# Performance work log

Hardware: AMD Instinct MI355X
Metric: run time of the kernel (lower is better)

Reference implementation:

```python
import jax, jax.numpy as jnp
import numpy as np

N_NODES = 100000
N_EDGES = 3200000
D_FEAT = 128
N1 = 128
N2 = 64
NUM_CLASSES = 10
NUM_GRAPHS = 256


def gcn_conv(x, edge_index, W, b, num_nodes):
    """PyG GCNConv: y = D^-1/2 (A+I) D^-1/2 (x W) + b, self-loops added."""
    src, dst = edge_index[0], edge_index[1]
    # degree including self-loop (edge weight 1)
    deg = jax.ops.segment_sum(jnp.ones_like(dst, dtype=x.dtype), dst,
                              num_segments=num_nodes) + 1.0
    dis = jnp.where(deg > 0, deg ** -0.5, 0.0)  # deg_inv_sqrt, [N]
    h = x @ W                                    # transform first, [N, out]
    norm = dis[src] * dis[dst]                   # [E]
    msg = h[src] * norm[:, None]                 # gather + scale, [E, out]
    agg = jax.ops.segment_sum(msg, dst, num_segments=num_nodes)
    agg = agg + h * (dis * dis)[:, None]         # self-loop contribution
    return agg + b


def global_mean_pool(x, batch, num_graphs):
    sums = jax.ops.segment_sum(x, batch, num_segments=num_graphs)
    cnt = jax.ops.segment_sum(jnp.ones((x.shape[0],), dtype=x.dtype), batch,
                              num_segments=num_graphs)
    return sums / jnp.maximum(cnt, 1.0)[:, None]


def setup_inputs() -> dict:
    key = jax.random.key(0)
    ks = jax.random.split(key, 8)
    x = jax.random.normal(ks[0], (N_NODES, D_FEAT), dtype=jnp.float32)
    edge_index = jax.random.randint(ks[1], (2, N_EDGES), 0, N_NODES, dtype=jnp.int64)
    batch = jnp.sort(jax.random.randint(ks[2], (N_NODES,), 0, NUM_GRAPHS, dtype=jnp.int64))
    W1 = jax.random.normal(ks[3], (D_FEAT, N1), dtype=jnp.float32) / np.sqrt(D_FEAT)
    b1 = jnp.zeros((N1,), dtype=jnp.float32)
    W2 = jax.random.normal(ks[4], (N1, N2), dtype=jnp.float32) / np.sqrt(N1)
    b2 = jnp.zeros((N2,), dtype=jnp.float32)
    Wfc = jax.random.normal(ks[5], (N2, NUM_CLASSES), dtype=jnp.float32) / np.sqrt(N2)
    bfc = jnp.zeros((NUM_CLASSES,), dtype=jnp.float32)
    return {"x": x, "edge_index": edge_index, "batch": batch,
            "W1": W1, "b1": b1, "W2": W2, "b2": b2,
            "Wfc": Wfc, "bfc": bfc, "num_graphs": NUM_GRAPHS}


def reference(x, edge_index, batch, W1, b1, W2, b2, Wfc, bfc, num_graphs):
    n = x.shape[0]
    h = gcn_conv(x, edge_index, W1, b1, n)
    h = jax.nn.relu(h)
    h = gcn_conv(h, edge_index, W2, b2, n)
    g = global_mean_pool(h, batch, num_graphs)   # [num_graphs, N2]
    # dropout is identity at inference
    return g @ Wfc + bfc                          # [num_graphs, num_classes]
```

## Files before the change

kernel.cpp:

```cpp
#include <hip/hip_runtime.h>
#include <math.h>

typedef unsigned int  u32;
typedef unsigned short u16;

#define TILE1 8192
#define BKW   256
#define CAP   9216

typedef __attribute__((ext_vector_type(8))) short bf16x8;
typedef __attribute__((ext_vector_type(4))) float f32x4;
union frag_u { bf16x8 v; u32 u[4]; uint4 q; };

__device__ inline u32 bf16_rne(float f) {
    u32 u = __float_as_uint(f);
    return (u + 0x7FFFu + ((u >> 16) & 1u)) >> 16;
}
__device__ inline float bf_lo(u32 u) { return __uint_as_float(u << 16); }
__device__ inline float bf_hi(u32 u) { return __uint_as_float(u & 0xFFFF0000u); }

__device__ inline void add8(float* acc, uint4 q) {
    acc[0] += bf_lo(q.x); acc[1] += bf_hi(q.x);
    acc[2] += bf_lo(q.y); acc[3] += bf_hi(q.y);
    acc[4] += bf_lo(q.z); acc[5] += bf_hi(q.z);
    acc[6] += bf_lo(q.w); acc[7] += bf_hi(q.w);
}

__device__ inline u32 relu_pk(u32 v) {
    u32 s = v & 0x80008000u;
    u32 m = (s >> 15) * 0xFFFFu;
    return v & ~m;
}


__global__ __launch_bounds__(512) void k_part1(const int* __restrict__ ei,
                                               int* __restrict__ bucketCur,
                                               u32* __restrict__ tmp,
                                               int E, int N, int NBK) {
    __shared__ int hist[1024];
    __shared__ int base[512];
    const int tid = threadIdx.x;
    if (tid < NBK) { hist[tid] = 0; hist[512 + tid] = 0; }
    __syncthreads();

    const int rep = (tid & 1) << 9;
    const int t0 = blockIdx.x * TILE1;
    const int4* ei4s = (const int4*)ei;
    const int4* ei4d = (const int4*)(ei + E);
    const int q0 = t0 >> 2;
    const int QE = E >> 2;

    int sv[16], dv[16], key[16];
#pragma unroll
    for (int j = 0; j < 4; ++j) {
        int qi = q0 + j * 512 + tid;
        int4 s4 = make_int4(0, 0, 0, 0), d4 = make_int4(-1, -1, -1, -1);
        if (qi < QE) { s4 = ei4s[qi]; d4 = ei4d[qi]; }
        sv[4 * j + 0] = s4.x; dv[4 * j + 0] = d4.x;
        sv[4 * j + 1] = s4.y; dv[4 * j + 1] = d4.y;
        sv[4 * j + 2] = s4.z; dv[4 * j + 2] = d4.z;
        sv[4 * j + 3] = s4.w; dv[4 * j + 3] = d4.w;
    }
#pragma unroll
    for (int j = 0; j < 16; ++j) {
        key[j] = -1;
        if ((unsigned)dv[j] < (unsigned)N && (unsigned)sv[j] < (unsigned)N) {
            key[j] = dv[j] >> 8;
            atomicAdd(&hist[key[j] + rep], 1);
        }
    }
    __syncthreads();
    if (tid < NBK) {
        int tot = hist[tid] + hist[512 + tid];
        base[tid] = atomicAdd(&bucketCur[tid], tot);
        hist[tid] = 0;
    }
    __syncthreads();
#pragma unroll
    for (int j = 0; j < 16; ++j) {
        if (key[j] >= 0) {
            int slot = atomicAdd(&hist[key[j]], 1);
            int off = base[key[j]] + slot;
            if (off < CAP)
                tmp[(size_t)key[j] * CAP + off] =
                    ((u32)(dv[j] & 255) << 17) | (u32)sv[j];
        }
    }
}

__global__ __launch_bounds__(512) void k_part2(const int* __restrict__ bucketCnt,
                                               const u32* __restrict__ tmp,
                                               int* __restrict__ csr,
                                               int* __restrict__ rowptr,
                                               float* __restrict__ dis,
                                               int N, int NBK) {
    __shared__ int hist[256];
    __shared__ int ts[512];
    __shared__ int sStart;
    const int b = blockIdx.x;
    const int t = threadIdx.x;

    int myCnt = (t < NBK) ? bucketCnt[t] : 0;
    ts[t] = myCnt;
    __syncthreads();
    for (int off = 1; off < 512; off <<= 1) {
        int u = (t >= off) ? ts[t - off] : 0;
        __syncthreads();
        ts[t] += u;
        __syncthreads();
    }
    if (t == b) sStart = ts[t] - myCnt;
    if (b == 0 && t == NBK - 1) rowptr[N] = ts[t];
    __syncthreads();
    const int start = sStart;
    const int cnt = bucketCnt[b];
    const u32* src = tmp + (size_t)b * CAP;

    if (t < 256) hist[t] = 0;
    __syncthreads();
    for (int i = t; i < cnt; i += 512)
        atomicAdd(&hist[src[i] >> 17], 1);
    __syncthreads();

    int h = (t < 256) ? hist[t] : 0;
    ts[t] = h;
    __syncthreads();
    for (int off = 1; off < 512; off <<= 1) {
        int u = (t >= off) ? ts[t - off] : 0;
        __syncthreads();
        ts[t] += u;
        __syncthreads();
    }
    if (t < 256) hist[t] = ts[t] - h;
    __syncthreads();

    if (t < 256) {
        int gn = (b << 8) + t;
        if (gn < N) {
            int e0 = hist[t];
            int e1 = (t < 255) ? hist[t + 1] : cnt;
            rowptr[gn] = start + e0;
            dis[gn] = rsqrtf((float)(e1 - e0) + 1.0f);
        }
    }
    __syncthreads();

    for (int i = t; i < cnt; i += 512) {
        u32 v = src[i];
        int p = atomicAdd(&hist[v >> 17], 1);
        csr[start + p] = (int)(v & 0x1FFFFu);
    }
}


__global__ __launch_bounds__(256) void k_convW(
    const float* __restrict__ W1, const float* __restrict__ W2,
    u32* __restrict__ W1h, u32* __restrict__ W1l,
    u32* __restrict__ W2h, u32* __restrict__ W2l,
    int* __restrict__ bucketCur, int NBK)
{
    int idx = blockIdx.x * 256 + threadIdx.x;
    if (idx < NBK) bucketCur[idx] = 0;
    if (idx < 8192) {
        int n = idx >> 6, k = (idx & 63) * 2;
        float w0 = W1[k * 128 + n], w1 = W1[(k + 1) * 128 + n];
        u32 h0 = bf16_rne(w0), h1 = bf16_rne(w1);
        u32 l0 = bf16_rne(w0 - __uint_as_float(h0 << 16));
        u32 l1 = bf16_rne(w1 - __uint_as_float(h1 << 16));
        W1h[idx] = h0 | (h1 << 16);
        W1l[idx] = l0 | (l1 << 16);
    } else if (idx < 12288) {
        int i2 = idx - 8192;
        int n = i2 >> 6, k = (i2 & 63) * 2;
        float w0 = W2[k * 64 + n], w1 = W2[(k + 1) * 64 + n];
        u32 h0 = bf16_rne(w0), h1 = bf16_rne(w1);
        u32 l0 = bf16_rne(w0 - __uint_as_float(h0 << 16));
        u32 l1 = bf16_rne(w1 - __uint_as_float(h1 << 16));
        W2h[i2] = h0 | (h1 << 16);
        W2l[i2] = l0 | (l1 << 16);
    }
}


__global__ __launch_bounds__(256) void k_gemm1m(
    const float* __restrict__ X, const u32* __restrict__ Wh,
    const u32* __restrict__ Wl, const float* __restrict__ dis,
    u32* __restrict__ Hb, int M)
{
    __shared__ uint4 sW[2176];
    const int tid = threadIdx.x;
    const int ny = blockIdx.y;
    const uint4* Wh4 = (const uint4*)Wh;
    const uint4* Wl4 = (const uint4*)Wl;
#pragma unroll
    for (int i = 0; i < 4; ++i) {
        int idx = tid + i * 256;
        int l = idx >> 4, j = idx & 15;
        sW[l * 17 + j] = Wh4[(ny * 64 + l) * 16 + j];
        sW[1088 + l * 17 + j] = Wl4[(ny * 64 + l) * 16 + j];
    }
    __syncthreads();

    const int w = tid >> 6, lane = tid & 63;
    const int mrow = blockIdx.x * 64 + w * 16;
    const int m16 = lane & 15, quad = lane >> 4;
    int gm = mrow + m16; if (gm >= M) gm = M - 1;

    frag_u Ah[4], Al[4];
    const float* xr = X + (size_t)gm * 128;
#pragma unroll
    for (int kt = 0; kt < 4; ++kt) {
        int kb = kt * 32 + quad * 8;
        float4 xa = *(const float4*)(xr + kb);
        float4 xb = *(const float4*)(xr + kb + 4);
        float xe[8] = {xa.x, xa.y, xa.z, xa.w, xb.x, xb.y, xb.z, xb.w};
#pragma unroll
        for (int j = 0; j < 4; ++j) {
            u32 h0 = bf16_rne(xe[2 * j]),     h1 = bf16_rne(xe[2 * j + 1]);
            u32 l0 = bf16_rne(xe[2 * j]     - __uint_as_float(h0 << 16));
            u32 l1 = bf16_rne(xe[2 * j + 1] - __uint_as_float(h1 << 16));
            Ah[kt].u[j] = h0 | (h1 << 16);
            Al[kt].u[j] = l0 | (l1 << 16);
        }
    }

    float dv[4];
#pragma unroll
    for (int r = 0; r < 4; ++r) {
        int gR = mrow + quad * 4 + r;
        dv[r] = (gR < M) ? dis[gR] : 0.f;
    }

#pragma unroll
    for (int nt = 0; nt < 4; ++nt) {
        f32x4 acc = {0.f, 0.f, 0.f, 0.f};
        int l = nt * 16 + m16;
#pragma unroll
        for (int kt = 0; kt < 4; ++kt) {
            frag_u Bh, Bl;
            Bh.q = sW[l * 17 + kt * 4 + quad];
            Bl.q = sW[1088 + l * 17 + kt * 4 + quad];
            acc = __builtin_amdgcn_mfma_f32_16x16x32_bf16(Al[kt].v, Bh.v, acc, 0, 0, 0);
            acc = __builtin_amdgcn_mfma_f32_16x16x32_bf16(Ah[kt].v, Bl.v, acc, 0, 0, 0);
            acc = __builtin_amdgcn_mfma_f32_16x16x32_bf16(Ah[kt].v, Bh.v, acc, 0, 0, 0);
        }
#pragma unroll
        for (int r = 0; r < 4; ++r) {
            float vs = acc[r] * dv[r];
            float vo = __shfl_xor(vs, 1, 64);
            if ((m16 & 1) == 0) {
                int gR = mrow + quad * 4 + r;
                if (gR < M)
                    Hb[(size_t)gR * 64 + ny * 32 + nt * 8 + (m16 >> 1)] =
                        bf16_rne(vs) | (bf16_rne(vo) << 16);
            }
        }
    }
}


__global__ __launch_bounds__(256) void k_gemm2m(
    const u32* __restrict__ Xb, const u32* __restrict__ Wh,
    const u32* __restrict__ Wl, const float* __restrict__ dis,
    u32* __restrict__ Hb, int M)
{
    __shared__ uint4 sW[2176];
    const int tid = threadIdx.x;
    const uint4* Wh4 = (const uint4*)Wh;
    const uint4* Wl4 = (const uint4*)Wl;
#pragma unroll
    for (int i = 0; i < 4; ++i) {
        int idx = tid + i * 256;
        int l = idx >> 4, j = idx & 15;
        sW[l * 17 + j] = Wh4[l * 16 + j];
        sW[1088 + l * 17 + j] = Wl4[l * 16 + j];
    }
    __syncthreads();

    const int w = tid >> 6, lane = tid & 63;
    const int mrow = blockIdx.x * 64 + w * 16;
    const int m16 = lane & 15, quad = lane >> 4;
    int gm = mrow + m16; if (gm >= M) gm = M - 1;

    const uint4* X4 = (const uint4*)Xb;
    frag_u A[4];
#pragma unroll
    for (int kt = 0; kt < 4; ++kt) {
        A[kt].q = X4[(size_t)gm * 16 + kt * 4 + quad];
#pragma unroll
        for (int j = 0; j < 4; ++j) A[kt].u[j] = relu_pk(A[kt].u[j]);
    }

    float dv[4];
#pragma unroll
    for (int r = 0; r < 4; ++r) {
        int gR = mrow + quad * 4 + r;
        dv[r] = (gR < M) ? dis[gR] : 0.f;
    }

#pragma unroll
    for (int nt = 0; nt < 4; ++nt) {
        f32x4 acc = {0.f, 0.f, 0.f, 0.f};
        int l = nt * 16 + m16;
#pragma unroll
        for (int kt = 0; kt < 4; ++kt) {
            frag_u Bh, Bl;
            Bh.q = sW[l * 17 + kt * 4 + quad];
            Bl.q = sW[1088 + l * 17 + kt * 4 + quad];
            acc = __builtin_amdgcn_mfma_f32_16x16x32_bf16(A[kt].v, Bl.v, acc, 0, 0, 0);
            acc = __builtin_amdgcn_mfma_f32_16x16x32_bf16(A[kt].v, Bh.v, acc, 0, 0, 0);
        }
#pragma unroll
        for (int r = 0; r < 4; ++r) {
            float vs = acc[r] * dv[r];
            float vo = __shfl_xor(vs, 1, 64);
            if ((m16 & 1) == 0) {
                int gR = mrow + quad * 4 + r;
                if (gR < M)
                    Hb[(size_t)gR * 32 + nt * 8 + (m16 >> 1)] =
                        bf16_rne(vs) | (bf16_rne(vo) << 16);
            }
        }
    }
}


template <int PART>
__global__ __launch_bounds__(256) void k_agg1h(
    const int* __restrict__ rowptr, const int* __restrict__ csr,
    const float* __restrict__ dis, const uint4* __restrict__ Hb4,
    const float* __restrict__ bias, u32* __restrict__ AGGb, int N)
{
    int n = (blockIdx.x * 256 + threadIdx.x) >> 6;
    int lane = threadIdx.x & 63;
    int slot = lane >> 3;
    int li   = lane & 7;
    if (n >= N) return;
    int e = rowptr[n];
    const int s1 = rowptr[n + 1];
    const float dn = dis[n];
    const int q = PART * 8 + li;

    float acc[8];
#pragma unroll
    for (int j = 0; j < 8; ++j) acc[j] = 0.f;

    for (; e + 16 <= s1; e += 16) {
        int i0 = csr[e + slot];
        int i1 = csr[e + 8 + slot];
        uint4 q0 = Hb4[(size_t)i0 * 16 + q];
        uint4 q1 = Hb4[(size_t)i1 * 16 + q];
        add8(acc, q0); add8(acc, q1);
    }
    for (; e + 8 <= s1; e += 8) {
        int i0 = csr[e + slot];
        uint4 q0 = Hb4[(size_t)i0 * 16 + q];
        add8(acc, q0);
    }
    {
        int rem = s1 - e;
        int idx = -1;
        if (slot < rem) idx = csr[e + slot];
        else if (slot == rem) idx = n;
        if (idx >= 0) {
            uint4 qq = Hb4[(size_t)idx * 16 + q];
            add8(acc, qq);
        }
    }

#pragma unroll
    for (int j = 0; j < 8; ++j) {
        acc[j] += __shfl_xor(acc[j], 8, 64);
        acc[j] += __shfl_xor(acc[j], 16, 64);
        acc[j] += __shfl_xor(acc[j], 32, 64);
    }

    if (slot < 2) {
        float4 bv = ((const float4*)bias)[q * 2 + slot];
        float o0 = fmaf(dn, acc[4 * slot + 0], bv.x);
        float o1 = fmaf(dn, acc[4 * slot + 1], bv.y);
        float o2 = fmaf(dn, acc[4 * slot + 2], bv.z);
        float o3 = fmaf(dn, acc[4 * slot + 3], bv.w);
        uint2 p;
        p.x = bf16_rne(o0) | (bf16_rne(o1) << 16);
        p.y = bf16_rne(o2) | (bf16_rne(o3) << 16);
        ((uint2*)AGGb)[(size_t)n * 32 + q * 2 + slot] = p;
    }
}


__global__ __launch_bounds__(256) void k_agg2(
    const int* __restrict__ rowptr, const int* __restrict__ csr,
    const float* __restrict__ dis, const uint4* __restrict__ Hb4,
    const float* __restrict__ bias, u32* __restrict__ AGGb, int N)
{
    int n = (blockIdx.x * 256 + threadIdx.x) >> 6;
    int lane = threadIdx.x & 63;
    int slot = lane >> 3;
    int li   = lane & 7;
    if (n >= N) return;
    int e = rowptr[n];
    const int s1 = rowptr[n + 1];
    const float dn = dis[n];

    float acc[8];
#pragma unroll
    for (int j = 0; j < 8; ++j) acc[j] = 0.f;

    for (; e + 16 <= s1; e += 16) {
        int i0 = csr[e + slot];
        int i1 = csr[e + 8 + slot];
        uint4 q0 = Hb4[(size_t)i0 * 8 + li];
        uint4 q1 = Hb4[(size_t)i1 * 8 + li];
        add8(acc, q0); add8(acc, q1);
    }
    for (; e + 8 <= s1; e += 8) {
        int i0 = csr[e + slot];
        uint4 q0 = Hb4[(size_t)i0 * 8 + li];
        add8(acc, q0);
    }
    {
        int rem = s1 - e;
        int idx = -1;
        if (slot < rem) idx = csr[e + slot];
        else if (slot == rem) idx = n;
        if (idx >= 0) {
            uint4 q = Hb4[(size_t)idx * 8 + li];
            add8(acc, q);
        }
    }

#pragma unroll
    for (int j = 0; j < 8; ++j) {
        acc[j] += __shfl_xor(acc[j], 8, 64);
        acc[j] += __shfl_xor(acc[j], 16, 64);
        acc[j] += __shfl_xor(acc[j], 32, 64);
    }

    if (slot < 2) {
        float4 bv = ((const float4*)bias)[li * 2 + slot];
        float o0 = fmaf(dn, acc[4 * slot + 0], bv.x);
        float o1 = fmaf(dn, acc[4 * slot + 1], bv.y);
        float o2 = fmaf(dn, acc[4 * slot + 2], bv.z);
        float o3 = fmaf(dn, acc[4 * slot + 3], bv.w);
        uint2 p;
        p.x = bf16_rne(o0) | (bf16_rne(o1) << 16);
        p.y = bf16_rne(o2) | (bf16_rne(o3) << 16);
        ((uint2*)AGGb)[(size_t)n * 16 + li * 2 + slot] = p;
    }
}


__device__ inline int lower_bound(const int* __restrict__ b, int n, int v) {
    int lo = 0, hi = n;
    while (lo < hi) { int m = (lo + hi) >> 1; if (b[m] < v) lo = m + 1; else hi = m; }
    return lo;
}

__global__ __launch_bounds__(256) void k_poolfc(
    const int* __restrict__ batch, const u32* __restrict__ AGGb2,
    const float* __restrict__ Wfc, const float* __restrict__ bfc,
    float* __restrict__ out, int n)
{
    int g = blockIdx.x;
    int start = lower_bound(batch, n, g);
    int end   = lower_bound(batch, n, g + 1);
    int tid = threadIdx.x;
    int f = tid & 63, stripe = tid >> 6;
    int ui = f >> 1, hi = f & 1;
    float acc = 0.f;
    for (int i = start + stripe; i < end; i += 4) {
        u32 v = AGGb2[(size_t)i * 32 + ui];
        acc += hi ? bf_hi(v) : bf_lo(v);
    }
    __shared__ float red[256];
    __shared__ float mean[64];
    red[tid] = acc;
    __syncthreads();
    if (tid < 64) {
        float s = red[tid] + red[tid + 64] + red[tid + 128] + red[tid + 192];
        float c = (float)(end - start);
        mean[tid] = s / fmaxf(c, 1.0f);
    }
    __syncthreads();
    if (tid < 10) {
        float o = bfc[tid];
        for (int k = 0; k < 64; ++k)
            o = fmaf(mean[k], Wfc[k * 10 + tid], o);
        out[g * 10 + tid] = o;
    }
}


extern "C" void kernel_launch(void* const* d_in, const int* in_sizes, int n_in,
                              void* d_out, int out_size, void* d_ws, size_t ws_size,
                              hipStream_t stream)
{
    const float* x    = (const float*)d_in[0];
    const int*   ei   = (const int*)d_in[1];
    const int*   batch= (const int*)d_in[2];
    const float* W1   = (const float*)d_in[3];
    const float* b1   = (const float*)d_in[4];
    const float* W2   = (const float*)d_in[5];
    const float* b2   = (const float*)d_in[6];
    const float* Wfc  = (const float*)d_in[7];
    const float* bfc  = (const float*)d_in[8];
    float* out = (float*)d_out;

    const int N  = in_sizes[0] / 128;
    const int E  = in_sizes[1] / 2;
    const int ng = out_size / 10;

    const int NBK = (N + BKW - 1) / BKW;

    int*   rowptr    = (int*)d_ws;
    int*   bucketCur = rowptr + 102400;
    float* dis       = (float*)(bucketCur + 512);
    int*   csr       = (int*)(dis + 102400);
    u32*   tmp       = (u32*)(csr + E);
    u32*   Hb1       = tmp;
    u32*   agg2b     = tmp;
    u32*   agg1b     = (u32*)((int*)tmp + (size_t)N * 64);
    u16*   Hb2       = (u16*)((int*)agg1b + (size_t)N * 128);
    u32*   W1h       = (u32*)((int*)Hb2 + (size_t)N * 32);
    u32*   W1l       = W1h + 8192;
    u32*   W2h       = W1l + 8192;
    u32*   W2l       = W2h + 4096;

    k_convW<<<48, 256, 0, stream>>>(W1, W2, W1h, W1l, W2h, W2l, bucketCur, NBK);
    k_part1<<<(E + TILE1 - 1) / TILE1, 512, 0, stream>>>(ei, bucketCur, tmp, E, N, NBK);
    k_part2<<<NBK, 512, 0, stream>>>(bucketCur, tmp, csr, rowptr, dis, N, NBK);

    k_gemm1m<<<dim3((N + 63) / 64, 2), 256, 0, stream>>>(x, W1h, W1l, dis, Hb1, N);
    k_agg1h<0><<<(N + 3) / 4, 256, 0, stream>>>(rowptr, csr, dis, (const uint4*)Hb1, b1, agg1b, N);
    k_agg1h<1><<<(N + 3) / 4, 256, 0, stream>>>(rowptr, csr, dis, (const uint4*)Hb1, b1, agg1b, N);

    k_gemm2m<<<(N + 63) / 64, 256, 0, stream>>>(agg1b, W2h, W2l, dis, (u32*)Hb2, N);
    k_agg2<<<(N + 3) / 4, 256, 0, stream>>>(rowptr, csr, dis, (const uint4*)Hb2, b2, agg2b, N);

    k_poolfc<<<ng, 256, 0, stream>>>(batch, agg2b, Wfc, bfc, out, N);
}
```

Baseline: 398.9 us.

## Widen GEMM1 to all output columns, swizzle LDS, deepen aggregation gather unroll

The first GEMM now has each block compute all 128 output columns, loading the whole split-bf16 W1 into LDS with an XOR swizzle instead of padding. X is read and converted once per row rather than once per half of the columns. The aggregation kernels unroll the neighbor gather to 32 edges per iteration, use 32-bit byte offsets instead of 64-bit indexing, make the row bounds wave-uniform with readfirstlane, and accumulate in packed float2 vectors. The changes trade more LDS per block and more registers in flight for fewer redundant loads and more memory-level parallelism, at some risk to occupancy.

```diff
diff --git a/kernel.cpp b/kernel.cpp
--- a/kernel.cpp
+++ b/kernel.cpp
@@ -10,6 +10,7 @@
 
 typedef __attribute__((ext_vector_type(8))) short bf16x8;
 typedef __attribute__((ext_vector_type(4))) float f32x4;
+typedef __attribute__((ext_vector_type(2))) float f32x2;
 union frag_u { bf16x8 v; u32 u[4]; uint4 q; };
 
 __device__ inline u32 bf16_rne(float f) {
@@ -19,11 +20,14 @@
 __device__ inline float bf_lo(u32 u) { return __uint_as_float(u << 16); }
 __device__ inline float bf_hi(u32 u) { return __uint_as_float(u & 0xFFFF0000u); }
 
-__device__ inline void add8(float* acc, uint4 q) {
-    acc[0] += bf_lo(q.x); acc[1] += bf_hi(q.x);
-    acc[2] += bf_lo(q.y); acc[3] += bf_hi(q.y);
-    acc[4] += bf_lo(q.z); acc[5] += bf_hi(q.z);
-    acc[6] += bf_lo(q.w); acc[7] += bf_hi(q.w);
+__device__ inline f32x2 up2(u32 u) {
+    f32x2 t;
+    t.x = __uint_as_float(u << 16);
+    t.y = __uint_as_float(u & 0xFFFF0000u);
+    return t;
+}
+__device__ inline void add8p(f32x2* a, uint4 q) {
+    a[0] += up2(q.x); a[1] += up2(q.y); a[2] += up2(q.z); a[3] += up2(q.w);
 }
 
 __device__ inline u32 relu_pk(u32 v) {
@@ -187,17 +191,17 @@
     const u32* __restrict__ Wl, const float* __restrict__ dis,
     u32* __restrict__ Hb, int M)
 {
-    __shared__ uint4 sW[2176];
+    __shared__ uint4 sW[4096];
     const int tid = threadIdx.x;
-    const int ny = blockIdx.y;
     const uint4* Wh4 = (const uint4*)Wh;
     const uint4* Wl4 = (const uint4*)Wl;
 #pragma unroll
-    for (int i = 0; i < 4; ++i) {
+    for (int i = 0; i < 8; ++i) {
         int idx = tid + i * 256;
         int l = idx >> 4, j = idx & 15;
-        sW[l * 17 + j] = Wh4[(ny * 64 + l) * 16 + j];
-        sW[1088 + l * 17 + j] = Wl4[(ny * 64 + l) * 16 + j];
+        int js = j ^ (l & 7);
+        sW[l * 16 + js] = Wh4[idx];
+        sW[2048 + l * 16 + js] = Wl4[idx];
     }
     __syncthreads();
 
@@ -232,14 +236,16 @@
     }
 
 #pragma unroll
-    for (int nt = 0; nt < 4; ++nt) {
+    for (int nt = 0; nt < 8; ++nt) {
         f32x4 acc = {0.f, 0.f, 0.f, 0.f};
         int l = nt * 16 + m16;
+        int swz = l & 7;
 #pragma unroll
         for (int kt = 0; kt < 4; ++kt) {
             frag_u Bh, Bl;
-            Bh.q = sW[l * 17 + kt * 4 + quad];
-            Bl.q = sW[1088 + l * 17 + kt * 4 + quad];
+            int jb = (kt * 4 + quad) ^ swz;
+            Bh.q = sW[l * 16 + jb];
+            Bl.q = sW[2048 + l * 16 + jb];
             acc = __builtin_amdgcn_mfma_f32_16x16x32_bf16(Al[kt].v, Bh.v, acc, 0, 0, 0);
             acc = __builtin_amdgcn_mfma_f32_16x16x32_bf16(Ah[kt].v, Bl.v, acc, 0, 0, 0);
             acc = __builtin_amdgcn_mfma_f32_16x16x32_bf16(Ah[kt].v, Bh.v, acc, 0, 0, 0);
@@ -251,7 +257,7 @@
             if ((m16 & 1) == 0) {
                 int gR = mrow + quad * 4 + r;
                 if (gR < M)
-                    Hb[(size_t)gR * 64 + ny * 32 + nt * 8 + (m16 >> 1)] =
+                    Hb[(size_t)gR * 64 + nt * 8 + (m16 >> 1)] =
                         bf16_rne(vs) | (bf16_rne(vo) << 16);
             }
         }
@@ -328,7 +334,7 @@
 template <int PART>
 __global__ __launch_bounds__(256) void k_agg1h(
     const int* __restrict__ rowptr, const int* __restrict__ csr,
-    const float* __restrict__ dis, const uint4* __restrict__ Hb4,
+    const float* __restrict__ dis, const u32* __restrict__ Hb,
     const float* __restrict__ bias, u32* __restrict__ AGGb, int N)
 {
     int n = (blockIdx.x * 256 + threadIdx.x) >> 6;
@@ -336,26 +342,40 @@
     int slot = lane >> 3;
     int li   = lane & 7;
     if (n >= N) return;
-    int e = rowptr[n];
-    const int s1 = rowptr[n + 1];
+    int e  = __builtin_amdgcn_readfirstlane(rowptr[n]);
+    int s1 = __builtin_amdgcn_readfirstlane(rowptr[n + 1]);
     const float dn = dis[n];
-    const int q = PART * 8 + li;
-
-    float acc[8];
-#pragma unroll
-    for (int j = 0; j < 8; ++j) acc[j] = 0.f;
-
+    const char* hb = (const char*)Hb;
+    const u32 offq = (u32)(PART * 128 + li * 16);
+
+    f32x2 acc[4];
+#pragma unroll
+    for (int j = 0; j < 4; ++j) acc[j] = 0.f;
+
+    for (; e + 32 <= s1; e += 32) {
+        const int* c = csr + e;
+        u32 b0 = (u32)c[slot]      << 8;
+        u32 b1 = (u32)c[8 + slot]  << 8;
+        u32 b2 = (u32)c[16 + slot] << 8;
+        u32 b3 = (u32)c[24 + slot] << 8;
+        uint4 q0 = *(const uint4*)(hb + b0 + offq);
+        uint4 q1 = *(const uint4*)(hb + b1 + offq);
+        uint4 q2 = *(const uint4*)(hb + b2 + offq);
+        uint4 q3 = *(const uint4*)(hb + b3 + offq);
+        add8p(acc, q0); add8p(acc, q1); add8p(acc, q2); add8p(acc, q3);
+    }
     for (; e + 16 <= s1; e += 16) {
-        int i0 = csr[e + slot];
-        int i1 = csr[e + 8 + slot];
-        uint4 q0 = Hb4[(size_t)i0 * 16 + q];
-        uint4 q1 = Hb4[(size_t)i1 * 16 + q];
-        add8(acc, q0); add8(acc, q1);
+        const int* c = csr + e;
+        u32 b0 = (u32)c[slot]     << 8;
+        u32 b1 = (u32)c[8 + slot] << 8;
+        uint4 q0 = *(const uint4*)(hb + b0 + offq);
+        uint4 q1 = *(const uint4*)(hb + b1 + offq);
+        add8p(acc, q0); add8p(acc, q1);
     }
     for (; e + 8 <= s1; e += 8) {
-        int i0 = csr[e + slot];
-        uint4 q0 = Hb4[(size_t)i0 * 16 + q];
-        add8(acc, q0);
+        u32 b0 = (u32)csr[e + slot] << 8;
+        uint4 q0 = *(const uint4*)(hb + b0 + offq);
+        add8p(acc, q0);
     }
     {
         int rem = s1 - e;
@@ -363,24 +383,28 @@
         if (slot < rem) idx = csr[e + slot];
         else if (slot == rem) idx = n;
         if (idx >= 0) {
-            uint4 qq = Hb4[(size_t)idx * 16 + q];
-            add8(acc, qq);
-        }
-    }
-
-#pragma unroll
-    for (int j = 0; j < 8; ++j) {
-        acc[j] += __shfl_xor(acc[j], 8, 64);
-        acc[j] += __shfl_xor(acc[j], 16, 64);
-        acc[j] += __shfl_xor(acc[j], 32, 64);
+            uint4 qq = *(const uint4*)(hb + ((u32)idx << 8) + offq);
+            add8p(acc, qq);
+        }
+    }
+
+#pragma unroll
+    for (int j = 0; j < 4; ++j) {
+        acc[j].x += __shfl_xor(acc[j].x, 8, 64);
+        acc[j].y += __shfl_xor(acc[j].y, 8, 64);
+        acc[j].x += __shfl_xor(acc[j].x, 16, 64);
+        acc[j].y += __shfl_xor(acc[j].y, 16, 64);
+        acc[j].x += __shfl_xor(acc[j].x, 32, 64);
+        acc[j].y += __shfl_xor(acc[j].y, 32, 64);
     }
 
     if (slot < 2) {
+        const int q = PART * 8 + li;
         float4 bv = ((const float4*)bias)[q * 2 + slot];
-        float o0 = fmaf(dn, acc[4 * slot + 0], bv.x);
-        float o1 = fmaf(dn, acc[4 * slot + 1], bv.y);
-        float o2 = fmaf(dn, acc[4 * slot + 2], bv.z);
-        float o3 = fmaf(dn, acc[4 * slot + 3], bv.w);
+        float o0 = fmaf(dn, acc[2 * slot + 0].x, bv.x);
+        float o1 = fmaf(dn, acc[2 * slot + 0].y, bv.y);
+        float o2 = fmaf(dn, acc[2 * slot + 1].x, bv.z);
+        float o3 = fmaf(dn, acc[2 * slot + 1].y, bv.w);
         uint2 p;
         p.x = bf16_rne(o0) | (bf16_rne(o1) << 16);
         p.y = bf16_rne(o2) | (bf16_rne(o3) << 16);
@@ -391,7 +415,7 @@
 
 __global__ __launch_bounds__(256) void k_agg2(
     const int* __restrict__ rowptr, const int* __restrict__ csr,
-    const float* __restrict__ dis, const uint4* __restrict__ Hb4,
+    const float* __restrict__ dis, const u32* __restrict__ Hb,
     const float* __restrict__ bias, u32* __restrict__ AGGb, int N)
 {
     int n = (blockIdx.x * 256 + threadIdx.x) >> 6;
@@ -399,25 +423,40 @@
     int slot = lane >> 3;
     int li   = lane & 7;
     if (n >= N) return;
-    int e = rowptr[n];
-    const int s1 = rowptr[n + 1];
+    int e  = __builtin_amdgcn_readfirstlane(rowptr[n]);
+    int s1 = __builtin_amdgcn_readfirstlane(rowptr[n + 1]);
     const float dn = dis[n];
-
-    float acc[8];
-#pragma unroll
-    for (int j = 0; j < 8; ++j) acc[j] = 0.f;
-
+    const char* hb = (const char*)Hb;
+    const u32 offq = (u32)li * 16u;
+
+    f32x2 acc[4];
+#pragma unroll
+    for (int j = 0; j < 4; ++j) acc[j] = 0.f;
+
+    for (; e + 32 <= s1; e += 32) {
+        const int* c = csr + e;
+        u32 b0 = (u32)c[slot]      << 7;
+        u32 b1 = (u32)c[8 + slot]  << 7;
+        u32 b2 = (u32)c[16 + slot] << 7;
+        u32 b3 = (u32)c[24 + slot] << 7;
+        uint4 q0 = *(const uint4*)(hb + b0 + offq);
+        uint4 q1 = *(const uint4*)(hb + b1 + offq);
+        uint4 q2 = *(const uint4*)(hb + b2 + offq);
+        uint4 q3 = *(const uint4*)(hb + b3 + offq);
+        add8p(acc, q0); add8p(acc, q1); add8p(acc, q2); add8p(acc, q3);
+    }
     for (; e + 16 <= s1; e += 16) {
-        int i0 = csr[e + slot];
-        int i1 = csr[e + 8 + slot];
-        uint4 q0 = Hb4[(size_t)i0 * 8 + li];
-        uint4 q1 = Hb4[(size_t)i1 * 8 + li];
-        add8(acc, q0); add8(acc, q1);
+        const int* c = csr + e;
+        u32 b0 = (u32)c[slot]     << 7;
+        u32 b1 = (u32)c[8 + slot] << 7;
+        uint4 q0 = *(const uint4*)(hb + b0 + offq);
+        uint4 q1 = *(const uint4*)(hb + b1 + offq);
+        add8p(acc, q0); add8p(acc, q1);
     }
     for (; e + 8 <= s1; e += 8) {
-        int i0 = csr[e + slot];
-        uint4 q0 = Hb4[(size_t)i0 * 8 + li];
-        add8(acc, q0);
+        u32 b0 = (u32)csr[e + slot] << 7;
+        uint4 q0 = *(const uint4*)(hb + b0 + offq);
+        add8p(acc, q0);
     }
     {
         int rem = s1 - e;
@@ -425,24 +464,27 @@
         if (slot < rem) idx = csr[e + slot];
         else if (slot == rem) idx = n;
         if (idx >= 0) {
-            uint4 q = Hb4[(size_t)idx * 8 + li];
-            add8(acc, q);
-        }
-    }
-
-#pragma unroll
-    for (int j = 0; j < 8; ++j) {
-        acc[j] += __shfl_xor(acc[j], 8, 64);
-        acc[j] += __shfl_xor(acc[j], 16, 64);
-        acc[j] += __shfl_xor(acc[j], 32, 64);
+            uint4 qq = *(const uint4*)(hb + ((u32)idx << 7) + offq);
+            add8p(acc, qq);
+        }
+    }
+
+#pragma unroll
+    for (int j = 0; j < 4; ++j) {
+        acc[j].x += __shfl_xor(acc[j].x, 8, 64);
+        acc[j].y += __shfl_xor(acc[j].y, 8, 64);
+        acc[j].x += __shfl_xor(acc[j].x, 16, 64);
+        acc[j].y += __shfl_xor(acc[j].y, 16, 64);
+        acc[j].x += __shfl_xor(acc[j].x, 32, 64);
+        acc[j].y += __shfl_xor(acc[j].y, 32, 64);
     }
 
     if (slot < 2) {
         float4 bv = ((const float4*)bias)[li * 2 + slot];
-        float o0 = fmaf(dn, acc[4 * slot + 0], bv.x);
-        float o1 = fmaf(dn, acc[4 * slot + 1], bv.y);
-        float o2 = fmaf(dn, acc[4 * slot + 2], bv.z);
-        float o3 = fmaf(dn, acc[4 * slot + 3], bv.w);
+        float o0 = fmaf(dn, acc[2 * slot + 0].x, bv.x);
+        float o1 = fmaf(dn, acc[2 * slot + 0].y, bv.y);
+        float o2 = fmaf(dn, acc[2 * slot + 1].x, bv.z);
+        float o3 = fmaf(dn, acc[2 * slot + 1].y, bv.w);
         uint2 p;
         p.x = bf16_rne(o0) | (bf16_rne(o1) << 16);
         p.y = bf16_rne(o2) | (bf16_rne(o3) << 16);
@@ -531,12 +573,12 @@
     k_part1<<<(E + TILE1 - 1) / TILE1, 512, 0, stream>>>(ei, bucketCur, tmp, E, N, NBK);
     k_part2<<<NBK, 512, 0, stream>>>(bucketCur, tmp, csr, rowptr, dis, N, NBK);
 
-    k_gemm1m<<<dim3((N + 63) / 64, 2), 256, 0, stream>>>(x, W1h, W1l, dis, Hb1, N);
-    k_agg1h<0><<<(N + 3) / 4, 256, 0, stream>>>(rowptr, csr, dis, (const uint4*)Hb1, b1, agg1b, N);
-    k_agg1h<1><<<(N + 3) / 4, 256, 0, stream>>>(rowptr, csr, dis, (const uint4*)Hb1, b1, agg1b, N);
+    k_gemm1m<<<(N + 63) / 64, 256, 0, stream>>>(x, W1h, W1l, dis, Hb1, N);
+    k_agg1h<0><<<(N + 3) / 4, 256, 0, stream>>>(rowptr, csr, dis, Hb1, b1, agg1b, N);
+    k_agg1h<1><<<(N + 3) / 4, 256, 0, stream>>>(rowptr, csr, dis, Hb1, b1, agg1b, N);
 
     k_gemm2m<<<(N + 63) / 64, 256, 0, stream>>>(agg1b, W2h, W2l, dis, (u32*)Hb2, N);
-    k_agg2<<<(N + 3) / 4, 256, 0, stream>>>(rowptr, csr, dis, (const uint4*)Hb2, b2, agg2b, N);
+    k_agg2<<<(N + 3) / 4, 256, 0, stream>>>(rowptr, csr, dis, (const u32*)Hb2, b2, agg2b, N);
 
     k_poolfc<<<ng, 256, 0, stream>>>(batch, agg2b, Wfc, bfc, out, N);
 }
```

After: 393.2 us. About the same (-1.4%).
